# Performance work log

Measured on AMD Instinct MI355X. Metric: run time of the kernel, lower is better.

The kernel has to match this reference:

```python
import jax, jax.numpy as jnp
import numpy as np

B, S, D, H = 2, 2048, 1024, 16
HD = D // H  # 64
EPS = 1e-8


def setup_inputs() -> dict:
    key = jax.random.key(0)
    ks = jax.random.split(key, 9)
    hidden_states = jax.random.normal(ks[0], (B, S, D), dtype=jnp.float32)
    # rotary tables: standard RoPE angles over half the head dim
    pos = jnp.arange(S, dtype=jnp.float32)[:, None]
    inv_freq = 1.0 / (10000.0 ** (jnp.arange(0, HD, 2, dtype=jnp.float32) / HD))  # [HD/2]
    ang = pos * inv_freq[None, :]  # [S, HD/2]
    sin = jnp.sin(ang)[None, None]  # [1,1,S,HD/2]
    cos = jnp.cos(ang)[None, None]
    s = 1.0 / np.sqrt(D)
    wq = jax.random.normal(ks[1], (D, D), dtype=jnp.float32) * s
    wk = jax.random.normal(ks[2], (D, D), dtype=jnp.float32) * s
    wv = jax.random.normal(ks[3], (D, D), dtype=jnp.float32) * s
    wo = jax.random.normal(ks[4], (D, D), dtype=jnp.float32) * s
    bo = jnp.zeros((D,), dtype=jnp.float32)
    scale = jnp.ones((D,), dtype=jnp.float32)
    return {"hidden_states": hidden_states, "sin": sin, "cos": cos,
            "wq": wq, "wk": wk, "wv": wv, "wo": wo, "bo": bo, "scale": scale}


def _heads(x):
    # [B,S,D] -> [B,H,S,HD]
    return x.reshape(B, S, H, HD).transpose(0, 2, 1, 3)


def _rotary(x, sin, cos):
    # interleaved RoPE: even/odd pairs
    x1, x2 = x[..., 0::2], x[..., 1::2]
    out = jnp.stack([x1 * cos - x2 * sin, x2 * cos + x1 * sin], axis=-1)
    return out.reshape(x.shape)


def reference(hidden_states, sin, cos, wq, wk, wv, wo, bo, scale):
    q = _rotary(_heads(hidden_states @ wq.T), sin, cos)
    k = _rotary(_heads(hidden_states @ wk.T), sin, cos)
    v = _rotary(_heads(hidden_states @ wv.T), sin, cos)
    scores = jnp.einsum("bhqd,bhkd->bhqk", q, k) / np.sqrt(HD)
    probs = jax.nn.softmax(scores, axis=-1)
    ctx = jnp.einsum("bhqk,bhkd->bhqd", probs, v)
    ctx = ctx.transpose(0, 2, 1, 3).reshape(B, S, D)
    out = ctx @ wo.T + bo
    x = out + hidden_states
    # RMSNorm: x / (||x||/sqrt(d) + eps) * scale
    rms = jnp.linalg.norm(x, axis=-1, keepdims=True) / np.sqrt(D)
    return scale * (x / (rms + EPS))
```

## Files before the change

kernel.cpp:

```cpp
#include <hip/hip_runtime.h>
#include <cmath>

#define BB 2
#define SS 2048
#define DD 1024
#define HH 16
#define HDIM 64
#define KDIM 1024
#define EPSF 1e-8f
#define QSCALE 0.18033688f

typedef __attribute__((ext_vector_type(8))) short bf16x8;
typedef __attribute__((ext_vector_type(4))) float f32x4;

__device__ __forceinline__ ushort f2bf(float x) {
    unsigned u = __builtin_bit_cast(unsigned, x);
    u += 0x7FFFu + ((u >> 16) & 1u);
    return (ushort)(u >> 16);
}

__device__ __forceinline__ void gload_lds16(const ushort* g, ushort* l) {
    __builtin_amdgcn_global_load_lds(
        (const __attribute__((address_space(1))) unsigned*)g,
        (__attribute__((address_space(3))) unsigned*)l, 16, 0, 0);
}

__global__ __launch_bounds__(256) void conv_bf16(
    const float* __restrict__ src, ushort* __restrict__ dst, int n4)
{
    const int i = blockIdx.x * 256 + threadIdx.x;
    if (i < n4) {
        const float4 v = ((const float4*)src)[i];
        ushort4 o;
        o.x = f2bf(v.x); o.y = f2bf(v.y); o.z = f2bf(v.z); o.w = f2bf(v.w);
        ((ushort4*)dst)[i] = o;
    }
}

__global__ __launch_bounds__(256) void gemm_qkv_mfma(
    const ushort* __restrict__ A,
    const ushort* __restrict__ Wq, const ushort* __restrict__ Wk,
    const ushort* __restrict__ Wv,
    const float* __restrict__ sinp, const float* __restrict__ cosp,
    ushort* __restrict__ Qb, ushort* __restrict__ Kb, ushort* __restrict__ Vtb)
{
    const int cb = blockIdx.y;
    const int z = cb >> 3;
    const int col0 = (cb & 7) * 128;
    const ushort* W = (z == 0) ? Wq : (z == 1) ? Wk : Wv;
    ushort* O = (z == 0) ? Qb : (z == 1) ? Kb : Vtb;
    const int row0 = blockIdx.x * 128;
    const float qs = (z == 0) ? QSCALE : 1.0f;

    __shared__ __align__(16) ushort As[128 * 32];
    __shared__ __align__(16) ushort Bs[128 * 32];

    const int tid = threadIdx.x;
    const int w = tid >> 6, lane = tid & 63;
    const int quad = lane >> 4, l15 = lane & 15;
    const int m_off = (w >> 1) * 64, n_off = (w & 1) * 64;

    f32x4 acc[4][4] = {};

    for (int k0 = 0; k0 < KDIM; k0 += 32) {
#pragma unroll
        for (int it = 0; it < 2; ++it) {
            const int L = (it * 4 + w) * 64 + lane;
            const int r = L >> 2, c8 = (L & 3) * 8;
            gload_lds16(A + (size_t)(row0 + r) * KDIM + k0 + c8, &As[L * 8]);
            gload_lds16(W + (size_t)(col0 + r) * KDIM + k0 + c8, &Bs[L * 8]);
        }
        __syncthreads();
        bf16x8 af[4], bfr[4];
#pragma unroll
        for (int i = 0; i < 4; ++i) {
            af[i]  = *(const bf16x8*)&As[(m_off + i * 16 + l15) * 32 + quad * 8];
            bfr[i] = *(const bf16x8*)&Bs[(n_off + i * 16 + l15) * 32 + quad * 8];
        }
#pragma unroll
        for (int i = 0; i < 4; ++i)
#pragma unroll
            for (int j = 0; j < 4; ++j)
                acc[i][j] = __builtin_amdgcn_mfma_f32_16x16x32_bf16(
                    af[i], bfr[j], acc[i][j], 0, 0, 0);
        __syncthreads();
    }

    const int b = (row0 + m_off) / SS;
#pragma unroll
    for (int mi = 0; mi < 4; ++mi) {
        const int mrow = row0 + m_off + mi * 16 + quad * 4;
#pragma unroll
        for (int ni = 0; ni < 4; ++ni) {
            const int c = col0 + n_off + ni * 16 + l15;
            const int h = c >> 6, e = c & 63;
            const int bh = b * HH + h;
            float outv[4];
#pragma unroll
            for (int r = 0; r < 4; ++r) {
                const int s = (mrow + r) & (SS - 1);
                const float sv = sinp[s * (HDIM / 2) + (e >> 1)];
                const float cv = cosp[s * (HDIM / 2) + (e >> 1)];
                const float v = acc[mi][ni][r];
                const float vp = __shfl_xor(v, 1);
                outv[r] = ((l15 & 1) ? (v * cv + vp * sv) : (v * cv - vp * sv)) * qs;
            }
            if (z < 2) {
#pragma unroll
                for (int r = 0; r < 4; ++r) {
                    const int s = (mrow + r) & (SS - 1);
                    const ushort mine = f2bf(outv[r]);
                    const ushort part = (ushort)__shfl_xor((int)mine, 1);
                    if (!(l15 & 1))
                        *(unsigned*)(O + ((size_t)(bh * SS + s)) * HDIM + e) =
                            (unsigned)mine | ((unsigned)part << 16);
                }
            } else {
                ushort4 pk;
                pk.x = f2bf(outv[0]); pk.y = f2bf(outv[1]);
                pk.z = f2bf(outv[2]); pk.w = f2bf(outv[3]);
                const int s0 = mrow & (SS - 1);
                *(ushort4*)(O + ((size_t)(bh * HDIM + e)) * SS + s0) = pk;
            }
        }
    }
}

__global__ __launch_bounds__(256) void attn_mfma(
    const ushort* __restrict__ Qb, const ushort* __restrict__ Kb,
    const ushort* __restrict__ Vtb, ushort* __restrict__ ctx)
{
    const int bh = blockIdx.y;
    const int b = bh / HH, h = bh % HH;
    const int q0 = blockIdx.x * 64;
    const int tid = threadIdx.x;
    const int w = tid >> 6;
    const int lane = tid & 63;
    const int quad = lane >> 4;
    const int l15 = lane & 15;

    __shared__ __align__(16) ushort kvs[8192];
    __shared__ __align__(16) float ps[64][68];

    const ushort* Qh = Qb  + (size_t)bh * SS * HDIM;
    const ushort* Kh = Kb  + (size_t)bh * SS * HDIM;
    const ushort* Vh = Vtb + (size_t)bh * HDIM * SS;

    const int qrow = q0 + w * 16 + l15;
    const bf16x8 qf0 = *(const bf16x8*)(Qh + (size_t)qrow * HDIM + quad * 8);
    const bf16x8 qf1 = *(const bf16x8*)(Qh + (size_t)qrow * HDIM + 32 + quad * 8);

    f32x4 cacc[4] = {{0,0,0,0},{0,0,0,0},{0,0,0,0},{0,0,0,0}};
    float lsum[4] = {0.f, 0.f, 0.f, 0.f};

    const int lr = lane >> 2;
    const int lc = (lane & 3) * 8;

    for (int k0 = 0; k0 < SS; k0 += 64) {
#pragma unroll
        for (int hf = 0; hf < 2; ++hf) {
            gload_lds16(Kh + (size_t)(k0 + w * 16 + lr) * HDIM + hf * 32 + lc,
                        &kvs[(hf * 64 + w * 16 + lr) * 32 + lc]);
            gload_lds16(Vh + (size_t)(w * 16 + lr) * SS + k0 + hf * 32 + lc,
                        &kvs[4096 + (hf * 64 + w * 16 + lr) * 32 + lc]);
        }
        __syncthreads();

        f32x4 sacc[4];
#pragma unroll
        for (int n0 = 0; n0 < 4; ++n0) {
            const bf16x8 kf0 = *(const bf16x8*)&kvs[(n0 * 16 + l15) * 32 + quad * 8];
            const bf16x8 kf1 = *(const bf16x8*)&kvs[(64 + n0 * 16 + l15) * 32 + quad * 8];
            f32x4 s = {0.f, 0.f, 0.f, 0.f};
            s = __builtin_amdgcn_mfma_f32_16x16x32_bf16(qf0, kf0, s, 0, 0, 0);
            s = __builtin_amdgcn_mfma_f32_16x16x32_bf16(qf1, kf1, s, 0, 0, 0);
            sacc[n0] = s;
        }

#pragma unroll
        for (int r = 0; r < 4; ++r) {
#pragma unroll
            for (int n0 = 0; n0 < 4; ++n0) {
                const float p = exp2f(sacc[n0][r]);
                ps[w * 16 + quad * 4 + r][n0 * 16 + l15] = p;
                lsum[r] += p;
            }
        }

#pragma unroll
        for (int step = 0; step < 2; ++step) {
            const float* pr = &ps[w * 16 + l15][step * 32 + quad * 8];
            const float4 p0 = *(const float4*)(pr);
            const float4 p1 = *(const float4*)(pr + 4);
            union { ushort us[8]; bf16x8 v; } pu;
            pu.us[0] = f2bf(p0.x); pu.us[1] = f2bf(p0.y);
            pu.us[2] = f2bf(p0.z); pu.us[3] = f2bf(p0.w);
            pu.us[4] = f2bf(p1.x); pu.us[5] = f2bf(p1.y);
            pu.us[6] = f2bf(p1.z); pu.us[7] = f2bf(p1.w);
#pragma unroll
            for (int d0 = 0; d0 < 4; ++d0) {
                const bf16x8 vf = *(const bf16x8*)&kvs[
                    4096 + (step * 64 + d0 * 16 + l15) * 32 + quad * 8];
                cacc[d0] = __builtin_amdgcn_mfma_f32_16x16x32_bf16(pu.v, vf, cacc[d0], 0, 0, 0);
            }
        }
        __syncthreads();
    }

#pragma unroll
    for (int r = 0; r < 4; ++r) {
#pragma unroll
        for (int off = 1; off < 16; off <<= 1) lsum[r] += __shfl_xor(lsum[r], off);
    }
    float inv[4];
#pragma unroll
    for (int r = 0; r < 4; ++r) inv[r] = 1.f / lsum[r];

#pragma unroll
    for (int d0 = 0; d0 < 4; ++d0)
#pragma unroll
        for (int r = 0; r < 4; ++r) {
            const int row = q0 + w * 16 + quad * 4 + r;
            ctx[((size_t)(b * SS + row)) * DD + h * HDIM + d0 * 16 + l15] =
                f2bf(cacc[d0][r] * inv[r]);
        }
}

__global__ __launch_bounds__(256) void gemm_out_mfma(
    const ushort* __restrict__ A, const ushort* __restrict__ W,
    const float* __restrict__ bias, float* __restrict__ Out)
{
    const int row0 = blockIdx.x * 128;
    const int col0 = blockIdx.y * 128;

    __shared__ __align__(16) ushort As[128 * 32];
    __shared__ __align__(16) ushort Bs[128 * 32];

    const int tid = threadIdx.x;
    const int w = tid >> 6, lane = tid & 63;
    const int quad = lane >> 4, l15 = lane & 15;
    const int m_off = (w >> 1) * 64, n_off = (w & 1) * 64;

    f32x4 acc[4][4] = {};

    for (int k0 = 0; k0 < KDIM; k0 += 32) {
#pragma unroll
        for (int it = 0; it < 2; ++it) {
            const int L = (it * 4 + w) * 64 + lane;
            const int r = L >> 2, c8 = (L & 3) * 8;
            gload_lds16(A + (size_t)(row0 + r) * KDIM + k0 + c8, &As[L * 8]);
            gload_lds16(W + (size_t)(col0 + r) * KDIM + k0 + c8, &Bs[L * 8]);
        }
        __syncthreads();
        bf16x8 af[4], bfr[4];
#pragma unroll
        for (int i = 0; i < 4; ++i) {
            af[i]  = *(const bf16x8*)&As[(m_off + i * 16 + l15) * 32 + quad * 8];
            bfr[i] = *(const bf16x8*)&Bs[(n_off + i * 16 + l15) * 32 + quad * 8];
        }
#pragma unroll
        for (int i = 0; i < 4; ++i)
#pragma unroll
            for (int j = 0; j < 4; ++j)
                acc[i][j] = __builtin_amdgcn_mfma_f32_16x16x32_bf16(
                    af[i], bfr[j], acc[i][j], 0, 0, 0);
        __syncthreads();
    }

#pragma unroll
    for (int mi = 0; mi < 4; ++mi) {
        const int mrow = row0 + m_off + mi * 16 + quad * 4;
#pragma unroll
        for (int ni = 0; ni < 4; ++ni) {
            const int c = col0 + n_off + ni * 16 + l15;
            const float bv = bias[c];
#pragma unroll
            for (int r = 0; r < 4; ++r)
                Out[(size_t)(mrow + r) * DD + c] = acc[mi][ni][r] + bv;
        }
    }
}

__global__ __launch_bounds__(256) void resid_rmsnorm(
    const float* __restrict__ proj, const float* __restrict__ hs,
    const float* __restrict__ scale, float* __restrict__ out)
{
    const int t = blockIdx.x;
    const int tid = threadIdx.x;
    const size_t base = (size_t)t * DD + tid * 4;

    const float4 p4 = *(const float4*)(proj + base);
    const float4 h4 = *(const float4*)(hs + base);
    float x0 = p4.x + h4.x, x1 = p4.y + h4.y, x2 = p4.z + h4.z, x3 = p4.w + h4.w;
    float ss = x0 * x0 + x1 * x1 + x2 * x2 + x3 * x3;

#pragma unroll
    for (int off = 1; off < 64; off <<= 1) ss += __shfl_xor(ss, off);

    __shared__ float wsum[4];
    if ((tid & 63) == 0) wsum[tid >> 6] = ss;
    __syncthreads();
    const float total = wsum[0] + wsum[1] + wsum[2] + wsum[3];
    const float inv = 1.f / (sqrtf(total * (1.f / DD)) + EPSF);

    const float4 s4 = *(const float4*)(scale + tid * 4);
    float4 o;
    o.x = s4.x * x0 * inv;
    o.y = s4.y * x1 * inv;
    o.z = s4.z * x2 * inv;
    o.w = s4.w * x3 * inv;
    *(float4*)(out + base) = o;
}

extern "C" void kernel_launch(void* const* d_in, const int* in_sizes, int n_in,
                              void* d_out, int out_size, void* d_ws, size_t ws_size,
                              hipStream_t stream) {
    const float* hs    = (const float*)d_in[0];
    const float* sinp  = (const float*)d_in[1];
    const float* cosp  = (const float*)d_in[2];
    const float* wq    = (const float*)d_in[3];
    const float* wk    = (const float*)d_in[4];
    const float* wv    = (const float*)d_in[5];
    const float* wo    = (const float*)d_in[6];
    const float* bo    = (const float*)d_in[7];
    const float* scale = (const float*)d_in[8];
    float* out = (float*)d_out;

    unsigned char* wsb = (unsigned char*)d_ws;
    const size_t MAT = (size_t)BB * SS * DD;
    const size_t WN  = (size_t)DD * DD;
    ushort* Abf = (ushort*)wsb;
    ushort* Wqb = Abf + MAT;
    ushort* Wkb = Wqb + WN;
    ushort* Wvb = Wkb + WN;
    ushort* Wob = Wvb + WN;
    ushort* Qb  = Wob + WN;
    ushort* Kb  = Qb + MAT;
    ushort* Vtb = Kb + MAT;
    ushort* ctxb = Vtb + MAT;
    float* proj = (float*)(ctxb + MAT);

    conv_bf16<<<dim3((int)(MAT / 4 / 256)), 256, 0, stream>>>(hs, Abf, (int)(MAT / 4));
    conv_bf16<<<dim3((int)(WN / 4 / 256)), 256, 0, stream>>>(wq, Wqb, (int)(WN / 4));
    conv_bf16<<<dim3((int)(WN / 4 / 256)), 256, 0, stream>>>(wk, Wkb, (int)(WN / 4));
    conv_bf16<<<dim3((int)(WN / 4 / 256)), 256, 0, stream>>>(wv, Wvb, (int)(WN / 4));
    conv_bf16<<<dim3((int)(WN / 4 / 256)), 256, 0, stream>>>(wo, Wob, (int)(WN / 4));

    gemm_qkv_mfma<<<dim3(32, 24), 256, 0, stream>>>(Abf, Wqb, Wkb, Wvb,
                                                    sinp, cosp, Qb, Kb, Vtb);
    attn_mfma<<<dim3(SS / 64, BB * HH), 256, 0, stream>>>(Qb, Kb, Vtb, ctxb);
    gemm_out_mfma<<<dim3(32, 8), 256, 0, stream>>>(ctxb, Wob, bo, proj);
    resid_rmsnorm<<<dim3(BB * SS), 256, 0, stream>>>(proj, hs, scale, out);
}
```

Before: 240.1 us.

## Rework attention to 32x32 MFMA with register-resident P and fuse conversions

The attention kernel moves from 16x16x32 to 32x32x16 bf16 MFMA with 128 query rows per block. S is computed transposed so the probabilities stay in registers and are repacked with cross-half shuffles, which removes the fp32 LDS round trip for P. P is now packed to bf16 by truncation instead of round-to-nearest, which adds a little bias. The five separate fp32-to-bf16 conversion launches are merged into one kernel to cut launch overhead.

```diff
diff --git a/kernel.cpp b/kernel.cpp
--- a/kernel.cpp
+++ b/kernel.cpp
@@ -12,6 +12,7 @@
 
 typedef __attribute__((ext_vector_type(8))) short bf16x8;
 typedef __attribute__((ext_vector_type(4))) float f32x4;
+typedef __attribute__((ext_vector_type(16))) float f32x16;
 
 __device__ __forceinline__ ushort f2bf(float x) {
     unsigned u = __builtin_bit_cast(unsigned, x);
@@ -19,22 +20,38 @@
     return (ushort)(u >> 16);
 }
 
+__device__ __forceinline__ unsigned pack_bf16_trunc(float a, float b) {
+    return __builtin_amdgcn_perm(__builtin_bit_cast(unsigned, b),
+                                 __builtin_bit_cast(unsigned, a), 0x07060302u);
+}
+
 __device__ __forceinline__ void gload_lds16(const ushort* g, ushort* l) {
     __builtin_amdgcn_global_load_lds(
         (const __attribute__((address_space(1))) unsigned*)g,
         (__attribute__((address_space(3))) unsigned*)l, 16, 0, 0);
 }
 
-__global__ __launch_bounds__(256) void conv_bf16(
-    const float* __restrict__ src, ushort* __restrict__ dst, int n4)
+__global__ __launch_bounds__(256) void conv_all(
+    const float* __restrict__ hs, const float* __restrict__ wq,
+    const float* __restrict__ wk, const float* __restrict__ wv,
+    const float* __restrict__ wo, ushort* __restrict__ dst)
 {
     const int i = blockIdx.x * 256 + threadIdx.x;
-    if (i < n4) {
-        const float4 v = ((const float4*)src)[i];
-        ushort4 o;
-        o.x = f2bf(v.x); o.y = f2bf(v.y); o.z = f2bf(v.z); o.w = f2bf(v.w);
-        ((ushort4*)dst)[i] = o;
-    }
+    const int HS4 = (BB * SS * DD) / 4;
+    const int W4 = (DD * DD) / 4;
+    const float* src;
+    int off;
+    if (i < HS4) { src = hs; off = i; }
+    else {
+        const int j = i - HS4;
+        const int seg = j / W4;
+        off = j - seg * W4;
+        src = (seg == 0) ? wq : (seg == 1) ? wk : (seg == 2) ? wv : wo;
+    }
+    const float4 v = ((const float4*)src)[off];
+    ushort4 o;
+    o.x = f2bf(v.x); o.y = f2bf(v.y); o.z = f2bf(v.z); o.w = f2bf(v.w);
+    ((ushort4*)dst)[i] = o;
 }
 
 __global__ __launch_bounds__(256) void gemm_qkv_mfma(
@@ -132,97 +149,103 @@
 {
     const int bh = blockIdx.y;
     const int b = bh / HH, h = bh % HH;
-    const int q0 = blockIdx.x * 64;
+    const int q0 = blockIdx.x * 128;
     const int tid = threadIdx.x;
     const int w = tid >> 6;
     const int lane = tid & 63;
-    const int quad = lane >> 4;
-    const int l15 = lane & 15;
-
-    __shared__ __align__(16) ushort kvs[8192];
-    __shared__ __align__(16) float ps[64][68];
+    const int l31 = lane & 31;
+    const int g = lane >> 5;
+
+    __shared__ __align__(16) ushort klds[4096];
+    __shared__ __align__(16) ushort vlds[4096];
 
     const ushort* Qh = Qb  + (size_t)bh * SS * HDIM;
     const ushort* Kh = Kb  + (size_t)bh * SS * HDIM;
     const ushort* Vh = Vtb + (size_t)bh * HDIM * SS;
 
-    const int qrow = q0 + w * 16 + l15;
-    const bf16x8 qf0 = *(const bf16x8*)(Qh + (size_t)qrow * HDIM + quad * 8);
-    const bf16x8 qf1 = *(const bf16x8*)(Qh + (size_t)qrow * HDIM + 32 + quad * 8);
-
-    f32x4 cacc[4] = {{0,0,0,0},{0,0,0,0},{0,0,0,0},{0,0,0,0}};
-    float lsum[4] = {0.f, 0.f, 0.f, 0.f};
+    const int qrow = q0 + w * 32 + l31;
+    bf16x8 qf[4];
+#pragma unroll
+    for (int ks = 0; ks < 4; ++ks)
+        qf[ks] = *(const bf16x8*)(Qh + (size_t)qrow * HDIM + ks * 16 + g * 8);
+
+    f32x16 cacc[2] = {};
+    float lsum = 0.f;
 
     const int lr = lane >> 2;
     const int lc = (lane & 3) * 8;
 
+    union U32x4 { unsigned u[4]; bf16x8 v; };
+
     for (int k0 = 0; k0 < SS; k0 += 64) {
 #pragma unroll
         for (int hf = 0; hf < 2; ++hf) {
             gload_lds16(Kh + (size_t)(k0 + w * 16 + lr) * HDIM + hf * 32 + lc,
-                        &kvs[(hf * 64 + w * 16 + lr) * 32 + lc]);
+                        &klds[(hf * 64 + w * 16 + lr) * 32 + lc]);
             gload_lds16(Vh + (size_t)(w * 16 + lr) * SS + k0 + hf * 32 + lc,
-                        &kvs[4096 + (hf * 64 + w * 16 + lr) * 32 + lc]);
-        }
-        __syncthreads();
-
-        f32x4 sacc[4];
-#pragma unroll
-        for (int n0 = 0; n0 < 4; ++n0) {
-            const bf16x8 kf0 = *(const bf16x8*)&kvs[(n0 * 16 + l15) * 32 + quad * 8];
-            const bf16x8 kf1 = *(const bf16x8*)&kvs[(64 + n0 * 16 + l15) * 32 + quad * 8];
-            f32x4 s = {0.f, 0.f, 0.f, 0.f};
-            s = __builtin_amdgcn_mfma_f32_16x16x32_bf16(qf0, kf0, s, 0, 0, 0);
-            s = __builtin_amdgcn_mfma_f32_16x16x32_bf16(qf1, kf1, s, 0, 0, 0);
-            sacc[n0] = s;
-        }
-
-#pragma unroll
-        for (int r = 0; r < 4; ++r) {
-#pragma unroll
-            for (int n0 = 0; n0 < 4; ++n0) {
-                const float p = exp2f(sacc[n0][r]);
-                ps[w * 16 + quad * 4 + r][n0 * 16 + l15] = p;
-                lsum[r] += p;
-            }
-        }
-
-#pragma unroll
-        for (int step = 0; step < 2; ++step) {
-            const float* pr = &ps[w * 16 + l15][step * 32 + quad * 8];
-            const float4 p0 = *(const float4*)(pr);
-            const float4 p1 = *(const float4*)(pr + 4);
-            union { ushort us[8]; bf16x8 v; } pu;
-            pu.us[0] = f2bf(p0.x); pu.us[1] = f2bf(p0.y);
-            pu.us[2] = f2bf(p0.z); pu.us[3] = f2bf(p0.w);
-            pu.us[4] = f2bf(p1.x); pu.us[5] = f2bf(p1.y);
-            pu.us[6] = f2bf(p1.z); pu.us[7] = f2bf(p1.w);
-#pragma unroll
-            for (int d0 = 0; d0 < 4; ++d0) {
-                const bf16x8 vf = *(const bf16x8*)&kvs[
-                    4096 + (step * 64 + d0 * 16 + l15) * 32 + quad * 8];
-                cacc[d0] = __builtin_amdgcn_mfma_f32_16x16x32_bf16(pu.v, vf, cacc[d0], 0, 0, 0);
-            }
-        }
-        __syncthreads();
-    }
-
-#pragma unroll
-    for (int r = 0; r < 4; ++r) {
-#pragma unroll
-        for (int off = 1; off < 16; off <<= 1) lsum[r] += __shfl_xor(lsum[r], off);
-    }
-    float inv[4];
-#pragma unroll
-    for (int r = 0; r < 4; ++r) inv[r] = 1.f / lsum[r];
-
-#pragma unroll
-    for (int d0 = 0; d0 < 4; ++d0)
-#pragma unroll
-        for (int r = 0; r < 4; ++r) {
-            const int row = q0 + w * 16 + quad * 4 + r;
-            ctx[((size_t)(b * SS + row)) * DD + h * HDIM + d0 * 16 + l15] =
-                f2bf(cacc[d0][r] * inv[r]);
+                        &vlds[(hf * 64 + w * 16 + lr) * 32 + lc]);
+        }
+        __syncthreads();
+
+        f32x16 sacc[2] = {};
+#pragma unroll
+        for (int kt = 0; kt < 2; ++kt)
+#pragma unroll
+            for (int ks = 0; ks < 4; ++ks) {
+                const bf16x8 kf = *(const bf16x8*)&klds[
+                    ((ks >> 1) * 64 + kt * 32 + l31) * 32 + (ks & 1) * 16 + g * 8];
+                sacc[kt] = __builtin_amdgcn_mfma_f32_32x32x16_bf16(
+                    kf, qf[ks], sacc[kt], 0, 0, 0);
+            }
+
+        unsigned pk[2][8];
+#pragma unroll
+        for (int kt = 0; kt < 2; ++kt)
+#pragma unroll
+            for (int i = 0; i < 8; ++i) {
+                const float pa = exp2f(sacc[kt][2 * i]);
+                const float pb = exp2f(sacc[kt][2 * i + 1]);
+                lsum += pa + pb;
+                pk[kt][i] = pack_bf16_trunc(pa, pb);
+            }
+
+#pragma unroll
+        for (int ks = 0; ks < 4; ++ks) {
+            const int kt = ks >> 1, bq = (ks & 1) * 4;
+            const unsigned s0 = (unsigned)__shfl_xor((int)pk[kt][bq + 0], 32);
+            const unsigned s1 = (unsigned)__shfl_xor((int)pk[kt][bq + 1], 32);
+            const unsigned s2 = (unsigned)__shfl_xor((int)pk[kt][bq + 2], 32);
+            const unsigned s3 = (unsigned)__shfl_xor((int)pk[kt][bq + 3], 32);
+            U32x4 pf;
+            pf.u[0] = g ? s2 : pk[kt][bq + 0];
+            pf.u[1] = g ? s3 : pk[kt][bq + 1];
+            pf.u[2] = g ? pk[kt][bq + 2] : s0;
+            pf.u[3] = g ? pk[kt][bq + 3] : s1;
+#pragma unroll
+            for (int dt = 0; dt < 2; ++dt) {
+                const bf16x8 vf = *(const bf16x8*)&vlds[
+                    ((ks >> 1) * 64 + dt * 32 + l31) * 32 + (ks & 1) * 16 + g * 8];
+                cacc[dt] = __builtin_amdgcn_mfma_f32_32x32x16_bf16(
+                    vf, pf.v, cacc[dt], 0, 0, 0);
+            }
+        }
+        __syncthreads();
+    }
+
+    lsum += __shfl_xor(lsum, 32);
+    const float inv = 1.f / lsum;
+
+    const size_t obase = ((size_t)(b * SS + qrow)) * DD + h * HDIM;
+#pragma unroll
+    for (int dt = 0; dt < 2; ++dt)
+#pragma unroll
+        for (int t = 0; t < 4; ++t) {
+            ushort4 o;
+            o.x = f2bf(cacc[dt][t * 4 + 0] * inv);
+            o.y = f2bf(cacc[dt][t * 4 + 1] * inv);
+            o.z = f2bf(cacc[dt][t * 4 + 2] * inv);
+            o.w = f2bf(cacc[dt][t * 4 + 3] * inv);
+            *(ushort4*)(ctx + obase + dt * 32 + t * 8 + g * 4) = o;
         }
 }
 
@@ -340,15 +363,12 @@
     ushort* ctxb = Vtb + MAT;
     float* proj = (float*)(ctxb + MAT);
 
-    conv_bf16<<<dim3((int)(MAT / 4 / 256)), 256, 0, stream>>>(hs, Abf, (int)(MAT / 4));
-    conv_bf16<<<dim3((int)(WN / 4 / 256)), 256, 0, stream>>>(wq, Wqb, (int)(WN / 4));
-    conv_bf16<<<dim3((int)(WN / 4 / 256)), 256, 0, stream>>>(wk, Wkb, (int)(WN / 4));
-    conv_bf16<<<dim3((int)(WN / 4 / 256)), 256, 0, stream>>>(wv, Wvb, (int)(WN / 4));
-    conv_bf16<<<dim3((int)(WN / 4 / 256)), 256, 0, stream>>>(wo, Wob, (int)(WN / 4));
+    const int nconv4 = (int)((MAT + 4 * WN) / 4);
+    conv_all<<<dim3(nconv4 / 256), 256, 0, stream>>>(hs, wq, wk, wv, wo, Abf);
 
     gemm_qkv_mfma<<<dim3(32, 24), 256, 0, stream>>>(Abf, Wqb, Wkb, Wvb,
                                                     sinp, cosp, Qb, Kb, Vtb);
-    attn_mfma<<<dim3(SS / 64, BB * HH), 256, 0, stream>>>(Qb, Kb, Vtb, ctxb);
+    attn_mfma<<<dim3(SS / 128, BB * HH), 256, 0, stream>>>(Qb, Kb, Vtb, ctxb);
     gemm_out_mfma<<<dim3(32, 8), 256, 0, stream>>>(ctxb, Wob, bo, proj);
     resid_rmsnorm<<<dim3(BB * SS), 256, 0, stream>>>(proj, hs, scale, out);
 }
```

New measurement: 230.1 us. 4.2% less time.
